# Kernel optimization log

Measured on AMD Instinct MI355X. Metric: run time of the kernel, lower is better.

## Reference

```python
import jax, jax.numpy as jnp
import numpy as np

D = 512      # embeddings_dim (in_features == out_features)
H = 4        # num_heads
MID = 2048   # mid_features
B, S = 4, 2048
EPS = 1e-5


def _ln(x, g, b):
    mu = jnp.mean(x, axis=-1, keepdims=True)
    var = jnp.mean(jnp.square(x - mu), axis=-1, keepdims=True)
    return g * (x - mu) / jnp.sqrt(var + EPS) + b


def setup_inputs() -> dict:
    key = jax.random.key(0)
    ks = jax.random.split(key, 16)
    w = 0.02  # weight init scale
    return {
        "x_encoder": jax.random.normal(ks[0], (B, S, D), jnp.float32),
        "x_decoder": jax.random.normal(ks[1], (B, S, D), jnp.float32),
        # per-head full-width projections (each head is a D->D Linear)
        "Wq": jax.random.normal(ks[2], (H, D, D), jnp.float32) * w,
        "bq": jnp.zeros((H, D), jnp.float32),
        "Wk": jax.random.normal(ks[3], (H, D, D), jnp.float32) * w,
        "bk": jnp.zeros((H, D), jnp.float32),
        "Wv": jax.random.normal(ks[4], (H, D, D), jnp.float32) * w,
        "bv": jnp.zeros((H, D), jnp.float32),
        # out_reshaper: Rearrange('b h s d -> b s (d h)') then Linear(D*H -> D)
        "Wo": jax.random.normal(ks[5], (D * H, D), jnp.float32) * w,
        "bo": jnp.zeros((D,), jnp.float32),
        "ln1_g": jnp.ones((D,), jnp.float32), "ln1_b": jnp.zeros((D,), jnp.float32),
        "ln2_g": jnp.ones((D,), jnp.float32), "ln2_b": jnp.zeros((D,), jnp.float32),
        # FouriFeedForward: D -> MID -> D with SELU
        "W1": jax.random.normal(ks[6], (D, MID), jnp.float32) * w,
        "b1": jnp.zeros((MID,), jnp.float32),
        "W2": jax.random.normal(ks[7], (MID, D), jnp.float32) * w,
        "b2": jnp.zeros((D,), jnp.float32),
        "ln3_g": jnp.ones((D,), jnp.float32), "ln3_b": jnp.zeros((D,), jnp.float32),
    }


def reference(x_encoder, x_decoder, Wq, bq, Wk, bk, Wv, bv, Wo, bo,
              ln1_g, ln1_b, ln2_g, ln2_b, W1, b1, W2, b2, ln3_g, ln3_b):
    # Fourier token mixing: per-batch fftn over (seq, feature) dims, keep real part
    xf = jnp.fft.fftn(x_decoder, axes=(1, 2)).real
    xd = _ln(x_decoder + xf, ln1_g, ln1_b)  # [B,S,D]

    # Linear multi-head attention: q from decoder, k/v from encoder.
    # qs/ks/vs: [B,H,S,D]; softmax over the HEAD axis (dim=1 in torch)
    qs = jax.nn.softmax(jnp.einsum('bsd,hde->bhse', xd, Wq) + bq[None, :, None, :], axis=1)
    ks = jax.nn.softmax(jnp.einsum('bsd,hde->bhse', x_encoder, Wk) + bk[None, :, None, :], axis=1)
    vs = jnp.einsum('bsd,hde->bhse', x_encoder, Wv) + bv[None, :, None, :]

    gc = jnp.einsum('bhsd,bhse->bhde', ks, vs)       # [B,H,D,D] global contexts
    out = jnp.einsum('bhsd,bhde->bhse', qs, gc)      # [B,H,S,D]

    # Rearrange 'b h s d -> b s (d h)': d is the slow axis, h the fast axis
    b, h, s, d = out.shape
    out = out.transpose(0, 2, 3, 1).reshape(b, s, d * h)
    attn = out @ Wo + bo                              # [B,S,D]

    x = _ln(xd + attn, ln2_g, ln2_b)
    ff = jax.nn.selu(x @ W1 + b1) @ W2 + b2           # dropout_p=0 (eval)
    x = _ln(x + ff, ln3_g, ln3_b)
    return x
```

## Files before the change

### kernel.cpp

```cpp
#include <hip/hip_runtime.h>
#include <stdint.h>

typedef __bf16 bf16;
typedef __bf16 bf16x8 __attribute__((ext_vector_type(8)));
typedef float f32x4 __attribute__((ext_vector_type(4)));

static __device__ __forceinline__ void async16(const void* g, void* l) {
  __builtin_amdgcn_global_load_lds(
      (__attribute__((address_space(1))) void*)g,
      (__attribute__((address_space(3))) void*)l, 16, 0, 0);
}

__global__ void __launch_bounds__(256) prep_all(
    const float* __restrict__ xdec, const float* __restrict__ xenc,
    bf16* __restrict__ Ttrig, bf16* __restrict__ Atrig2,
    bf16* __restrict__ xdec_b, bf16* __restrict__ xenc_b,
    const float* __restrict__ Wq, const float* __restrict__ Wk,
    const float* __restrict__ Wv, const float* __restrict__ Wo,
    const float* __restrict__ W1, const float* __restrict__ W2,
    bf16* __restrict__ BtQ, bf16* __restrict__ BtK, bf16* __restrict__ BtV,
    bf16* __restrict__ WoTh, bf16* __restrict__ W1T, bf16* __restrict__ W2T) {
  __shared__ bf16 tile[32][33];
  int id = blockIdx.x;
  if (id < 512) {
    int idx = id * 256 + threadIdx.x;
    int d0 = (idx & 127) * 4, jp = idx >> 7;
    int jj = jp >> 1, p = jp & 1;
    bf16 o[4] __attribute__((aligned(8)));
#pragma unroll
    for (int i = 0; i < 4; ++i) {
      int tt = ((d0 + i) * jj) & 511;
      float ang = (float)tt * (6.283185307179586f / 512.0f);
      o[i] = (bf16)(p ? __sinf(ang) : __cosf(ang));
    }
    *(uint2*)(Ttrig + jp * 512 + d0) = *(const uint2*)o;
  } else if (id < 2960) {
    int idx = (id - 512) * 256 + threadIdx.x;
    int k0 = (idx % 272) * 4;
    int rr = idx / 272;
    int r = rr % 1152, half = rr / 1152;
    bf16 o[4] __attribute__((aligned(8)));
#pragma unroll
    for (int i = 0; i < 4; ++i) {
      int k = k0 + i;
      float v = 0.0f;
      int tt = (r * k) & 2047;
      float ang = (float)tt * (6.283185307179586f / 2048.0f);
      if (half == 0) { if (r <= 1024 && k <= 1024) v = __cosf(ang); }
      else           { if (r <= 1023 && k >= 1 && k <= 1023) v = -__sinf(ang); }
      o[i] = (bf16)v;
    }
    *(uint2*)(Atrig2 + (long)rr * 1088 + k0) = *(const uint2*)o;
  } else if (id < 7056) {
    int i = ((id - 2960) * 256 + threadIdx.x) * 4;
    float4 v = *(const float4*)(xdec + i);
    bf16 o[4] __attribute__((aligned(8))) =
        {(bf16)v.x, (bf16)v.y, (bf16)v.z, (bf16)v.w};
    *(uint2*)(xdec_b + i) = *(const uint2*)o;
  } else if (id < 11152) {
    int i = ((id - 7056) * 256 + threadIdx.x) * 4;
    float4 v = *(const float4*)(xenc + i);
    bf16 o[4] __attribute__((aligned(8))) =
        {(bf16)v.x, (bf16)v.y, (bf16)v.z, (bf16)v.w};
    *(uint2*)(xenc_b + i) = *(const uint2*)o;
  } else {
    int id2 = id - 11152;
    int kind = id2 >> 10, t = id2 & 1023;
    const float* in; bf16* out; int R, C, rt, ct;
    bool iperm = false, hsel = false; int hh = 0;
    if (kind == 0)      { in = Wq; out = BtQ; R = 2048; C = 512; rt = t >> 4; ct = t & 15; iperm = true; }
    else if (kind == 1) { in = Wk; out = BtK; R = 2048; C = 512; rt = t >> 4; ct = t & 15; iperm = true; }
    else if (kind == 2) { in = Wv; out = BtV; R = 2048; C = 512; rt = t >> 4; ct = t & 15; iperm = true; }
    else if (kind == 3) {
      int zz = t >> 8, tt = t & 255;
      in = Wo; out = WoTh + (long)zz * 262144;
      R = 512; C = 512; rt = tt >> 4; ct = tt & 15; hsel = true; hh = zz;
    }
    else if (kind == 4) { in = W1; out = W1T; R = 512; C = 2048; rt = t >> 6; ct = t & 63; }
    else                { in = W2; out = W2T; R = 2048; C = 512; rt = t >> 4; ct = t & 15; }
    int c0 = ct * 32, r0 = rt * 32;
    int tx = threadIdx.x & 31, ty = threadIdx.x >> 5;
#pragma unroll
    for (int i = 0; i < 32; i += 8) {
      int r = r0 + ty + i;
      int rr = hsel ? (4 * r + hh) : r;
      tile[ty + i][tx] = (bf16)in[(long)rr * C + (c0 + tx)];
    }
    __syncthreads();
#pragma unroll
    for (int i = 0; i < 32; i += 8) {
      int cc = c0 + ty + i, rr = r0 + tx;
      if (iperm) {
        int e = cc, h = rr >> 9;
        int n = (e & 15) | (h << 4) | ((e >> 4) << 6);
        out[((long)n << 9) + (rr & 511)] = tile[tx][ty + i];
      } else {
        out[(long)cc * R + rr] = tile[tx][ty + i];
      }
    }
  }
}

__global__ void __launch_bounds__(256) fold_y(const bf16* __restrict__ Yt,
                                              bf16* __restrict__ Yf2) {
  int idx = blockIdx.x * 256 + threadIdx.x;
  int k0 = (idx % 272) * 4;
  int rr = idx / 272;
  int j = rr & 511, z = rr >> 9;
  int b = z & 3, half = z >> 2;
  const bf16* yin = Yt + (long)b * 2097152 + (long)j * 4096;
  bf16 o[4] __attribute__((aligned(8)));
  if (half == 0) {
    bf16 f[4] __attribute__((aligned(8)));
    *(uint2*)f = *(const uint2*)(yin + k0);
#pragma unroll
    for (int i = 0; i < 4; ++i) {
      int k = k0 + i;
      float v;
      if (k == 0)            v = (float)f[0];
      else if (k == 1024)    v = (float)f[i];
      else if (k < 1024)     v = (float)f[i] + (float)yin[2048 - k];
      else                   v = 0.0f;
      o[i] = (bf16)v;
    }
  } else {
    bf16 f[4] __attribute__((aligned(8)));
    *(uint2*)f = *(const uint2*)(yin + 2048 + k0);
#pragma unroll
    for (int i = 0; i < 4; ++i) {
      int k = k0 + i;
      float v = 0.0f;
      if (k >= 1 && k <= 1023) v = (float)f[i] - (float)yin[4096 - k];
      o[i] = (bf16)v;
    }
  }
  *(uint2*)(Yf2 + (long)z * 557056 + (long)j * 1088 + k0) = *(const uint2*)o;
}

__global__ void __launch_bounds__(256) ln1_kernel(
    const float* __restrict__ xdec, const bf16* __restrict__ CSb,
    const float* __restrict__ g, const float* __restrict__ be,
    bf16* __restrict__ outb) {
  const int row = blockIdx.x, t = threadIdx.x;
  const int b = row >> 11, s = row & 2047;
  const int sp = (s <= 1024) ? s : 2048 - s;
  const float sgn = (s <= 1024) ? 1.0f : -1.0f;
  const bf16* Crow = CSb + ((long)b * 1152 + sp) * 512;
  const bf16* Srow = CSb + ((long)(b + 4) * 1152 + sp) * 512;
  const long base = (long)row * 512;
  float2 xp = *(const float2*)(xdec + base + 2 * t);
  bf16 cp[2] __attribute__((aligned(4)));
  bf16 spv[2] __attribute__((aligned(4)));
  *(uint*)cp = *(const uint*)(Crow + 2 * t);
  *(uint*)spv = *(const uint*)(Srow + 2 * t);
  float v0 = xp.x + (float)cp[0] + sgn * (float)spv[0];
  float v1 = xp.y + (float)cp[1] + sgn * (float)spv[1];
  float sm = v0 + v1, q = v0 * v0 + v1 * v1;
#pragma unroll
  for (int off = 32; off > 0; off >>= 1) {
    sm += __shfl_down(sm, off);
    q += __shfl_down(q, off);
  }
  __shared__ float red[8];
  const int wv = t >> 6, ln = t & 63;
  if (ln == 0) { red[wv] = sm; red[wv + 4] = q; }
  __syncthreads();
  float S = red[0] + red[1] + red[2] + red[3];
  float Q = red[4] + red[5] + red[6] + red[7];
  float mu = S * (1.0f / 512.0f);
  float var = Q * (1.0f / 512.0f) - mu * mu;
  float rstd = rsqrtf(var + 1e-5f);
  float2 gp = *(const float2*)(g + 2 * t);
  float2 bp = *(const float2*)(be + 2 * t);
  bf16 op[2] __attribute__((aligned(4)));
  op[0] = (bf16)(gp.x * (v0 - mu) * rstd + bp.x);
  op[1] = (bf16)(gp.y * (v1 - mu) * rstd + bp.y);
  *(uint*)(outb + base + 2 * t) = *(const uint*)op;
}

template <int WRITE_BF16, int WRITE_F32>
__global__ void __launch_bounds__(256) ln_kernel(
    const bf16* __restrict__ A, const bf16* __restrict__ Bv,
    const float* __restrict__ g, const float* __restrict__ be,
    bf16* __restrict__ outb, float* __restrict__ outf) {
  const int row = blockIdx.x, t = threadIdx.x;
  const long base = (long)row * 512;
  bf16 ap[2] __attribute__((aligned(4)));
  bf16 bpv[2] __attribute__((aligned(4)));
  *(uint*)ap = *(const uint*)(A + base + 2 * t);
  *(uint*)bpv = *(const uint*)(Bv + base + 2 * t);
  float v0 = (float)ap[0] + (float)bpv[0];
  float v1 = (float)ap[1] + (float)bpv[1];
  float s = v0 + v1, q = v0 * v0 + v1 * v1;
#pragma unroll
  for (int off = 32; off > 0; off >>= 1) {
    s += __shfl_down(s, off);
    q += __shfl_down(q, off);
  }
  __shared__ float red[8];
  const int wv = t >> 6, ln = t & 63;
  if (ln == 0) { red[wv] = s; red[wv + 4] = q; }
  __syncthreads();
  float S = red[0] + red[1] + red[2] + red[3];
  float Q = red[4] + red[5] + red[6] + red[7];
  float mu = S * (1.0f / 512.0f);
  float var = Q * (1.0f / 512.0f) - mu * mu;
  float rstd = rsqrtf(var + 1e-5f);
  float2 gp = *(const float2*)(g + 2 * t);
  float2 bp = *(const float2*)(be + 2 * t);
  float o0 = gp.x * (v0 - mu) * rstd + bp.x;
  float o1 = gp.y * (v1 - mu) * rstd + bp.y;
  if (WRITE_BF16) {
    bf16 op[2] __attribute__((aligned(4)));
    op[0] = (bf16)o0; op[1] = (bf16)o1;
    *(uint*)(outb + base + 2 * t) = *(const uint*)op;
  }
  if (WRITE_F32) {
    float2 of; of.x = o0; of.y = o1;
    *(float2*)(outf + base + 2 * t) = of;
  }
}

template <int BN, int ADDR_MODE, int HAS_BIAS, int DO_SELU, int F32OUT, int SWIZ,
          int AHEAD>
static __device__ __forceinline__ void gemm_bt_body(
    int id, bf16* lA, bf16* lB,
    const bf16* __restrict__ A, const bf16* __restrict__ Bt,
    const float* __restrict__ bias, void* __restrict__ Cout,
    int N, int K, long sAz, long sBz, long sBiasz, long sCz,
    int gx, int gy, int gin) {
  int x, y, z;
  {
    if (SWIZ == 0) {
      x = id % gx; int t2 = id / gx; y = t2 % gy; z = t2 / gy;
    } else {
      int xcd = id & 7, r = id >> 3;
      int inner = r % gin, G = xcd + 8 * (r / gin);
      if (SWIZ == 1)      { y = G; x = inner % gx; z = inner / gx; }
      else if (SWIZ == 2) { z = G; x = inner % gx; y = inner / gx; }
      else                { x = G; y = inner % gy; z = inner / gy; }
    }
  }
  A  += (AHEAD == 1) ? sAz * (z & 3) : (AHEAD == 2) ? sAz * (z >> 2) : sAz * z;
  Bt += sBz * z;
  const int m0 = y * 128, n0 = x * BN;
  const int t = threadIdx.x;
  const int lane = t & 63, wave = t >> 6;
  const int srow = t >> 3;
  const int pch  = t & 7;
  const int lch  = pch ^ (srow & 7);
  const bf16* Ag = A  + (long)(m0 + srow) * K + lch * 8;
  const bf16* Bg = Bt + (long)(n0 + srow) * K + lch * 8;
  bf16* lAp = lA + srow * 64 + pch * 8;
  bf16* lBp = lB + srow * 64 + pch * 8;
  constexpr int MI = (BN == 128) ? 4 : 2;
  const int wm = (BN == 128) ? (wave >> 1) * 64 : wave * 32;
  const int wn = (BN == 128) ? (wave & 1) * 64 : 0;
  const int fr = lane & 15, fq = lane >> 4;

  f32x4 acc[MI][4] = {};

  for (int k0 = 0; k0 < K; k0 += 64) {
    __syncthreads();
#pragma unroll
    for (int i = 0; i < 4; ++i)
      async16(Ag + k0 + (long)(32 * i) * K, lAp + 32 * i * 64);
#pragma unroll
    for (int i = 0; i < BN / 32; ++i)
      async16(Bg + k0 + (long)(32 * i) * K, lBp + 32 * i * 64);
    __syncthreads();
#pragma unroll
    for (int kk = 0; kk < 2; ++kk) {
      bf16x8 av[MI], bfrag[4];
#pragma unroll
      for (int mi = 0; mi < MI; ++mi) {
        int r = wm + mi * 16 + fr;
        int c = (kk * 4 + fq) ^ (r & 7);
        av[mi] = *(const bf16x8*)&lA[r * 64 + c * 8];
      }
#pragma unroll
      for (int ni = 0; ni < 4; ++ni) {
        int r = wn + ni * 16 + fr;
        int c = (kk * 4 + fq) ^ (r & 7);
        bfrag[ni] = *(const bf16x8*)&lB[r * 64 + c * 8];
      }
#pragma unroll
      for (int mi = 0; mi < MI; ++mi)
#pragma unroll
        for (int ni = 0; ni < 4; ++ni)
          acc[mi][ni] = __builtin_amdgcn_mfma_f32_16x16x32_bf16(
              av[mi], bfrag[ni], acc[mi][ni], 0, 0, 0);
    }
  }

#pragma unroll
  for (int mi = 0; mi < MI; ++mi) {
#pragma unroll
    for (int ni = 0; ni < 4; ++ni) {
      const int col = n0 + wn + ni * 16 + fr;
      float bias_v = 0.0f;
      if (HAS_BIAS == 1) bias_v = bias[sBiasz * z + col];
      if (ADDR_MODE == 9) {
        const int b = z >> 2, h = z & 3;
        const int kidx = (col & 15) | (h << 4) | ((col >> 4) << 6);
#pragma unroll
        for (int r = 0; r < 4; ++r) {
          const int row = m0 + wm + mi * 16 + fq * 4 + r;
          ((bf16*)Cout)[((long)(b * 512 + row)) * 2048 + kidx] =
              (bf16)(acc[mi][ni][r] + bias_v);
        }
      } else {
#pragma unroll
        for (int r = 0; r < 4; ++r) {
          const int row = m0 + wm + mi * 16 + fq * 4 + r;
          float v = acc[mi][ni][r] + bias_v;
          if (DO_SELU) v = v > 0.0f ? 1.0507009873554805f * v
                                    : 1.7580993408473766f * (__expf(v) - 1.0f);
          long addr = sCz * z + (long)row * N + col;
          if (F32OUT) ((float*)Cout)[addr] = v;
          else        ((bf16*)Cout)[addr] = (bf16)v;
        }
      }
    }
  }
}

template <int BN, int ADDR_MODE, int HAS_BIAS, int DO_SELU, int F32OUT, int SWIZ,
          int AHEAD = 0>
__global__ void __launch_bounds__(256, 2) gemm_bt(
    const bf16* __restrict__ A, const bf16* __restrict__ Bt,
    const float* __restrict__ bias, void* __restrict__ Cout,
    int N, int K, long sAz, long sBz, long sBiasz, long sCz,
    int gx, int gy, int gin) {
  __shared__ __align__(16) bf16 lA[128 * 64];
  __shared__ __align__(16) bf16 lB[BN * 64];
  gemm_bt_body<BN, ADDR_MODE, HAS_BIAS, DO_SELU, F32OUT, SWIZ, AHEAD>(
      blockIdx.x, lA, lB, A, Bt, bias, Cout, N, K, sAz, sBz, sBiasz, sCz, gx, gy, gin);
}

static __device__ __forceinline__ void qkv_body(
    int id, bf16* lA, bf16* lB,
    const bf16* __restrict__ Aq, const bf16* __restrict__ Aenc,
    const bf16* __restrict__ BQ, const bf16* __restrict__ BK,
    const bf16* __restrict__ BV,
    const float* __restrict__ bq, const float* __restrict__ bk,
    const float* __restrict__ bv,
    bf16* __restrict__ qs2, bf16* __restrict__ ksT, bf16* __restrict__ vsT) {
  const int sid = id & 1023;
  const int xcd = sid & 7, r = sid >> 3;
  const int x = r & 15, y = xcd + 8 * (r >> 4);
  const bf16 *A = Aq, *Bt = BQ; bf16* out = qs2; const float* bias = bq;
  (void)Aenc; (void)BK; (void)BV; (void)bk; (void)bv; (void)ksT; (void)vsT;
  const int K = 512;
  const int m0 = y * 128, n0 = x * 128;
  const int t = threadIdx.x;
  const int lane = t & 63, wave = t >> 6;
  const int srow = t >> 3, pch = t & 7, lch = pch ^ (srow & 7);
  const bf16* Ag = A  + (long)(m0 + srow) * K + lch * 8;
  const bf16* Bg = Bt + (long)(n0 + srow) * K + lch * 8;
  bf16* lAp = lA + srow * 64 + pch * 8;
  bf16* lBp = lB + srow * 64 + pch * 8;
  const int wm = (wave >> 1) * 64, wn = (wave & 1) * 64;
  const int fr = lane & 15, fq = lane >> 4;

  f32x4 acc[4][4] = {};
  for (int k0 = 0; k0 < K; k0 += 64) {
    __syncthreads();
#pragma unroll
    for (int i = 0; i < 4; ++i) {
      async16(Ag + k0 + (long)(32 * i) * K, lAp + 32 * i * 64);
      async16(Bg + k0 + (long)(32 * i) * K, lBp + 32 * i * 64);
    }
    __syncthreads();
#pragma unroll
    for (int kk = 0; kk < 2; ++kk) {
      bf16x8 av[4], bfrag[4];
#pragma unroll
      for (int mi = 0; mi < 4; ++mi) {
        int rr = wm + mi * 16 + fr;
        int c = (kk * 4 + fq) ^ (rr & 7);
        av[mi] = *(const bf16x8*)&lA[rr * 64 + c * 8];
      }
#pragma unroll
      for (int ni = 0; ni < 4; ++ni) {
        int rr = wn + ni * 16 + fr;
        int c = (kk * 4 + fq) ^ (rr & 7);
        bfrag[ni] = *(const bf16x8*)&lB[rr * 64 + c * 8];
      }
#pragma unroll
      for (int mi = 0; mi < 4; ++mi)
#pragma unroll
        for (int ni = 0; ni < 4; ++ni)
          acc[mi][ni] = __builtin_amdgcn_mfma_f32_16x16x32_bf16(
              av[mi], bfrag[ni], acc[mi][ni], 0, 0, 0);
    }
  }

  const int ebase = fr + 16 * ((n0 + wn) >> 6);
  const float b0 = bias[ebase], b1 = bias[512 + ebase],
              b2 = bias[1024 + ebase], b3 = bias[1536 + ebase];
#pragma unroll
  for (int mi = 0; mi < 4; ++mi) {
#pragma unroll
    for (int r = 0; r < 4; ++r) {
      const int row = m0 + wm + mi * 16 + fq * 4 + r;
      float v0 = acc[mi][0][r] + b0;
      float v1 = acc[mi][1][r] + b1;
      float v2 = acc[mi][2][r] + b2;
      float v3 = acc[mi][3][r] + b3;
      float m = fmaxf(fmaxf(v0, v1), fmaxf(v2, v3));
      float p0 = __expf(v0 - m), p1 = __expf(v1 - m),
            p2 = __expf(v2 - m), p3 = __expf(v3 - m);
      float rs = 1.0f / (p0 + p1 + p2 + p3);
      const long ob = (long)row * 2048 + n0 + wn + fr;
      out[ob]      = (bf16)(p0 * rs);
      out[ob + 16] = (bf16)(p1 * rs);
      out[ob + 32] = (bf16)(p2 * rs);
      out[ob + 48] = (bf16)(p3 * rs);
    }
  }
}

static __device__ __forceinline__ void kv2_body(
    int sid, bf16* smem,
    const bf16* __restrict__ Aenc, const bf16* __restrict__ BK,
    const bf16* __restrict__ BV,
    const float* __restrict__ bk, const float* __restrict__ bv,
    bf16* __restrict__ ksT, bf16* __restrict__ vsT) {
  const int xcd = sid & 7, r = sid >> 3;
  const int x = r & 15, y = xcd + 8 * (r >> 4);
  const int K = 512;
  const int m0 = y * 128, n0 = x * 128;
  const int t = threadIdx.x;
  const int lane = t & 63, wave = t >> 6;
  const int srow = t >> 3, pch = t & 7, lch = pch ^ (srow & 7);
  bf16* lA  = smem;
  bf16* lBK = smem + 8192;
  bf16* lBV = smem + 16384;
  const bf16* Ag  = Aenc + (long)(m0 + srow) * K + lch * 8;
  const bf16* BKg = BK   + (long)(n0 + srow) * K + lch * 8;
  const bf16* BVg = BV   + (long)(n0 + srow) * K + lch * 8;
  bf16* lAp  = lA  + srow * 64 + pch * 8;
  bf16* lBKp = lBK + srow * 64 + pch * 8;
  bf16* lBVp = lBV + srow * 64 + pch * 8;
  const int wm = (wave >> 1) * 64, wn = (wave & 1) * 64;
  const int fr = lane & 15, fq = lane >> 4;

  f32x4 accK[4][4] = {}, accV[4][4] = {};
  for (int k0 = 0; k0 < K; k0 += 64) {
    __syncthreads();
#pragma unroll
    for (int i = 0; i < 4; ++i) {
      async16(Ag  + k0 + (long)(32 * i) * K, lAp  + 32 * i * 64);
      async16(BKg + k0 + (long)(32 * i) * K, lBKp + 32 * i * 64);
      async16(BVg + k0 + (long)(32 * i) * K, lBVp + 32 * i * 64);
    }
    __syncthreads();
#pragma unroll
    for (int kk = 0; kk < 2; ++kk) {
      bf16x8 av[4], bkf[4], bvf[4];
#pragma unroll
      for (int mi = 0; mi < 4; ++mi) {
        int rr = wm + mi * 16 + fr;
        int c = (kk * 4 + fq) ^ (rr & 7);
        av[mi] = *(const bf16x8*)&lA[rr * 64 + c * 8];
      }
#pragma unroll
      for (int ni = 0; ni < 4; ++ni) {
        int rr = wn + ni * 16 + fr;
        int c = (kk * 4 + fq) ^ (rr & 7);
        bkf[ni] = *(const bf16x8*)&lBK[rr * 64 + c * 8];
        bvf[ni] = *(const bf16x8*)&lBV[rr * 64 + c * 8];
      }
#pragma unroll
      for (int mi = 0; mi < 4; ++mi)
#pragma unroll
        for (int ni = 0; ni < 4; ++ni) {
          accK[mi][ni] = __builtin_amdgcn_mfma_f32_16x16x32_bf16(
              av[mi], bkf[ni], accK[mi][ni], 0, 0, 0);
          accV[mi][ni] = __builtin_amdgcn_mfma_f32_16x16x32_bf16(
              av[mi], bvf[ni], accV[mi][ni], 0, 0, 0);
        }
    }
  }

  const int ebase = fr + 16 * ((n0 + wn) >> 6);
  const float kb0 = bk[ebase], kb1 = bk[512 + ebase],
              kb2 = bk[1024 + ebase], kb3 = bk[1536 + ebase];
  const float vb0 = bv[ebase], vb1 = bv[512 + ebase],
              vb2 = bv[1024 + ebase], vb3 = bv[1536 + ebase];
  bf16* lT = smem;
  const int bb = m0 >> 11;
  const int s_tile = m0 & 2047;
  const int e_loc = fr + 16 * (wn >> 6);
  const int c = lane & 15, rg = lane >> 4;

  __syncthreads();
#pragma unroll
  for (int mi = 0; mi < 4; ++mi) {
    const int s0 = wm + mi * 16 + fq * 4;
    bf16 tmp[4][4] __attribute__((aligned(8)));
#pragma unroll
    for (int r2 = 0; r2 < 4; ++r2) {
      float v0 = accK[mi][0][r2] + kb0;
      float v1 = accK[mi][1][r2] + kb1;
      float v2 = accK[mi][2][r2] + kb2;
      float v3 = accK[mi][3][r2] + kb3;
      float m = fmaxf(fmaxf(v0, v1), fmaxf(v2, v3));
      float p0 = __expf(v0 - m), p1 = __expf(v1 - m),
            p2 = __expf(v2 - m), p3 = __expf(v3 - m);
      float rs = 1.0f / (p0 + p1 + p2 + p3);
      tmp[0][r2] = (bf16)(p0 * rs); tmp[1][r2] = (bf16)(p1 * rs);
      tmp[2][r2] = (bf16)(p2 * rs); tmp[3][r2] = (bf16)(p3 * rs);
    }
#pragma unroll
    for (int ni = 0; ni < 4; ++ni) {
      const int row = ni * 32 + e_loc;
      const int el = row * 128 + ((((s0 >> 3) ^ (row & 15)) << 3) | (s0 & 7));
      *(uint2*)&lT[el] = *(const uint2*)tmp[ni];
    }
  }
  __syncthreads();
#pragma unroll
  for (int i = 0; i < 8; ++i) {
    const int row = wave * 32 + rg + i * 4;
    const int el = row * 128 + ((c ^ (row & 15)) << 3);
    uint4 v = *(const uint4*)&lT[el];
    const int h = row >> 5, e = (row & 31) + 32 * x;
    *(uint4*)(ksT + ((long)((bb * 4 + h) * 512 + e)) * 2048 + s_tile + c * 8) = v;
  }

  __syncthreads();
#pragma unroll
  for (int mi = 0; mi < 4; ++mi) {
    const int s0 = wm + mi * 16 + fq * 4;
    bf16 tmp[4][4] __attribute__((aligned(8)));
#pragma unroll
    for (int r2 = 0; r2 < 4; ++r2) {
      tmp[0][r2] = (bf16)(accV[mi][0][r2] + vb0);
      tmp[1][r2] = (bf16)(accV[mi][1][r2] + vb1);
      tmp[2][r2] = (bf16)(accV[mi][2][r2] + vb2);
      tmp[3][r2] = (bf16)(accV[mi][3][r2] + vb3);
    }
#pragma unroll
    for (int ni = 0; ni < 4; ++ni) {
      const int row = ni * 32 + e_loc;
      const int el = row * 128 + ((((s0 >> 3) ^ (row & 15)) << 3) | (s0 & 7));
      *(uint2*)&lT[el] = *(const uint2*)tmp[ni];
    }
  }
  __syncthreads();
#pragma unroll
  for (int i = 0; i < 8; ++i) {
    const int row = wave * 32 + rg + i * 4;
    const int el = row * 128 + ((c ^ (row & 15)) << 3);
    uint4 v = *(const uint4*)&lT[el];
    const int h = row >> 5, e = (row & 31) + 32 * x;
    *(uint4*)(vsT + ((long)((bb * 4 + h) * 512 + e)) * 2048 + s_tile + c * 8) = v;
  }
}

__global__ void __launch_bounds__(256, 2) fused_kv_yt(
    const bf16* __restrict__ Aenc, const bf16* __restrict__ BK,
    const bf16* __restrict__ BV,
    const float* __restrict__ bk, const float* __restrict__ bv,
    bf16* __restrict__ ksT, bf16* __restrict__ vsT,
    const bf16* __restrict__ Ttrig, const bf16* __restrict__ xdec_b,
    bf16* __restrict__ Yt) {
  __shared__ __align__(16) bf16 smem[24576];
  int id = blockIdx.x;
  if (id < 1024)
    kv2_body(id, smem, Aenc, BK, BV, bk, bv, ksT, vsT);
  else
    gemm_bt_body<128, 0, 0, 0, 0, 3, 0>(id - 1024, smem, smem + 8192,
        Ttrig, xdec_b, nullptr, Yt, 2048, 512, 0L, 1048576L, 0L, 2097152L, 16, 8, 32);
}

__global__ void __launch_bounds__(256, 2) fused_gc_cs(
    const bf16* __restrict__ ksT, const bf16* __restrict__ vsT,
    bf16* __restrict__ gc,
    const bf16* __restrict__ Atrig2, const bf16* __restrict__ Yf2,
    bf16* __restrict__ CSb) {
  __shared__ __align__(16) bf16 smem[12288];
  int id = blockIdx.x;
  if (id < 512)
    gemm_bt_body<64, 0, 0, 0, 0, 2, 0>(id, smem, smem + 8192,
        ksT, vsT, nullptr, gc, 512, 2048, 1048576L, 1048576L, 0L, 262144L, 8, 4, 32);
  else
    gemm_bt_body<64, 0, 0, 0, 0, 2, 2>(id - 512, smem, smem + 8192,
        Atrig2, Yf2, nullptr, CSb, 512, 1088, 1253376L, 557056L, 0L, 589824L, 8, 9, 72);
}

__global__ void __launch_bounds__(256, 2) fused_q_gw(
    const bf16* __restrict__ Aq, const bf16* __restrict__ BQ,
    const float* __restrict__ bq, bf16* __restrict__ qs2,
    const bf16* __restrict__ WoTh, const bf16* __restrict__ gc,
    bf16* __restrict__ gwT) {
  __shared__ __align__(16) bf16 smem[16384];
  int id = blockIdx.x;
  if (id < 1024)
    qkv_body(id, smem, smem + 8192, Aq, nullptr, BQ, nullptr, nullptr,
             bq, nullptr, nullptr, qs2, nullptr, nullptr);
  else
    gemm_bt_body<64, 9, 0, 0, 0, 2, 1>(id - 1024, smem, smem + 8192,
        WoTh, gc, nullptr, gwT, 512, 512, 262144L, 262144L, 0L, 0L, 8, 4, 32);
}

extern "C" void kernel_launch(void* const* d_in, const int* in_sizes, int n_in,
                              void* d_out, int out_size, void* d_ws, size_t ws_size,
                              hipStream_t stream) {
  (void)in_sizes; (void)n_in; (void)out_size; (void)ws_size;
  const float* x_enc = (const float*)d_in[0];
  const float* x_dec = (const float*)d_in[1];
  const float* Wq = (const float*)d_in[2];
  const float* bq = (const float*)d_in[3];
  const float* Wk = (const float*)d_in[4];
  const float* bk = (const float*)d_in[5];
  const float* Wv = (const float*)d_in[6];
  const float* bv = (const float*)d_in[7];
  const float* Wo = (const float*)d_in[8];
  const float* bo = (const float*)d_in[9];
  const float* g1 = (const float*)d_in[10];
  const float* be1 = (const float*)d_in[11];
  const float* g2 = (const float*)d_in[12];
  const float* be2 = (const float*)d_in[13];
  const float* W1 = (const float*)d_in[14];
  const float* b1 = (const float*)d_in[15];
  const float* W2 = (const float*)d_in[16];
  const float* b2 = (const float*)d_in[17];
  const float* g3 = (const float*)d_in[18];
  const float* be3 = (const float*)d_in[19];

  char* ws = (char*)d_ws;
  const size_t MB = 1u << 20;
  bf16*  BtQ    = (bf16*) (ws + 0);
  bf16*  midb   = (bf16*) (ws + 0);
  bf16*  ksT    = (bf16*) (ws + 32 * MB);
  bf16*  attn_b = (bf16*) (ws + 32 * MB);
  bf16*  vsT    = (bf16*) (ws + 64 * MB);
  bf16*  ff_b   = (bf16*) (ws + 72 * MB);
  bf16*  Atrig2 = (bf16*) (ws + 96 * MB);
  bf16*  Ttrig  = (bf16*) (ws + 101 * MB);
  bf16*  CSb    = (bf16*) (ws + 102 * MB);
  bf16*  qs2    = (bf16*) (ws + 96 * MB);
  bf16*  xenc_b = (bf16*) (ws + 128 * MB);
  bf16*  BtK    = (bf16*) (ws + 136 * MB);
  bf16*  BtV    = (bf16*) (ws + 138 * MB);
  bf16*  xd_b   = (bf16*) (ws + 192 * MB);
  bf16*  x2_b   = (bf16*) (ws + 200 * MB);
  bf16*  gwT    = (bf16*) (ws + 208 * MB);
  bf16*  Yt     = (bf16*) (ws + 216 * MB);
  bf16*  gc     = (bf16*) (ws + 216 * MB);
  bf16*  Yf2    = (bf16*) (ws + 232 * MB);
  bf16*  WoTh   = (bf16*) (ws + 241 * MB);
  bf16*  W1T    = (bf16*) (ws + 243 * MB);
  bf16*  W2T    = (bf16*) (ws + 245 * MB);
  bf16*  xdec_b = (bf16*) (ws + 247 * MB);

  prep_all<<<17296, 256, 0, stream>>>(x_dec, x_enc, Ttrig, Atrig2, xdec_b, xenc_b,
                                      Wq, Wk, Wv, Wo, W1, W2,
                                      BtQ, BtK, BtV, WoTh, W1T, W2T);

  fused_kv_yt<<<1536, 256, 0, stream>>>(xenc_b, BtK, BtV, bk, bv, ksT, vsT,
                                        Ttrig, xdec_b, Yt);

  fold_y<<<4352, 256, 0, stream>>>(Yt, Yf2);

  fused_gc_cs<<<1088, 256, 0, stream>>>(ksT, vsT, gc, Atrig2, Yf2, CSb);

  ln1_kernel<<<8192, 256, 0, stream>>>(x_dec, CSb, g1, be1, xd_b);

  fused_q_gw<<<1536, 256, 0, stream>>>(xd_b, BtQ, bq, qs2, WoTh, gc, gwT);

  gemm_bt<64, 0, 1, 0, 0, 1><<<512, 256, 0, stream>>>(
      qs2, gwT, bo, attn_b, 512, 2048, 4194304L, 1048576L, 0L, 1048576L, 8, 16, 32);
  ln_kernel<1, 0><<<8192, 256, 0, stream>>>(
      xd_b, attn_b, g2, be2, x2_b, nullptr);

  gemm_bt<128, 0, 1, 1, 0, 1><<<1024, 256, 0, stream>>>(
      x2_b, W1T, b1, midb, 2048, 512, 0L, 0L, 0L, 0L, 16, 64, 16);
  gemm_bt<64, 0, 1, 0, 0, 1><<<512, 256, 0, stream>>>(
      midb, W2T, b2, ff_b, 512, 2048, 0L, 0L, 0L, 0L, 8, 64, 8);
  ln_kernel<0, 1><<<8192, 256, 0, stream>>>(
      x2_b, ff_b, g3, be3, nullptr, (float*)d_out);
}
```

Measured before the change: 355.6 us.

## Split-K the two K=2048 output GEMMs and sum the partials in LayerNorm

Replaces the attention output projection and FFN down-projection GEMMs (K=2048, N=512) with a split-K kernel. It uses 128x128 tiles, divides K into two halves and writes fp32 partial sums to two buffers. The following LayerNorm kernels read both partials and add them to the residual, so no separate reduction pass is needed. The aim is more work per block and better CU utilisation on a small N. The cost is extra fp32 write and read traffic and uncoalesced scalar stores in the epilogue.

```diff
diff --git a/kernel.cpp b/kernel.cpp
--- a/kernel.cpp
+++ b/kernel.cpp
@@ -179,18 +179,19 @@
 }
 
 template <int WRITE_BF16, int WRITE_F32>
-__global__ void __launch_bounds__(256) ln_kernel(
-    const bf16* __restrict__ A, const bf16* __restrict__ Bv,
+__global__ void __launch_bounds__(256) ln_sum2(
+    const bf16* __restrict__ A, const float* __restrict__ P0,
+    const float* __restrict__ P1,
     const float* __restrict__ g, const float* __restrict__ be,
     bf16* __restrict__ outb, float* __restrict__ outf) {
   const int row = blockIdx.x, t = threadIdx.x;
   const long base = (long)row * 512;
   bf16 ap[2] __attribute__((aligned(4)));
-  bf16 bpv[2] __attribute__((aligned(4)));
   *(uint*)ap = *(const uint*)(A + base + 2 * t);
-  *(uint*)bpv = *(const uint*)(Bv + base + 2 * t);
-  float v0 = (float)ap[0] + (float)bpv[0];
-  float v1 = (float)ap[1] + (float)bpv[1];
+  float2 p0 = *(const float2*)(P0 + base + 2 * t);
+  float2 p1 = *(const float2*)(P1 + base + 2 * t);
+  float v0 = (float)ap[0] + p0.x + p1.x;
+  float v1 = (float)ap[1] + p0.y + p1.y;
   float s = v0 + v1, q = v0 * v0 + v1 * v1;
 #pragma unroll
   for (int off = 32; off > 0; off >>= 1) {
@@ -338,19 +339,106 @@
       blockIdx.x, lA, lB, A, Bt, bias, Cout, N, K, sAz, sBz, sBiasz, sCz, gx, gy, gin);
 }
 
+template <int Z4>
+__global__ void __launch_bounds__(256, 2) gemm_sk2(
+    const bf16* __restrict__ A, const bf16* __restrict__ Bt,
+    const float* __restrict__ bias,
+    float* __restrict__ P0, float* __restrict__ P1,
+    long sAz, long sBz) {
+  __shared__ __align__(16) bf16 lA[128 * 64];
+  __shared__ __align__(16) bf16 lB[2][64 * 64];
+  const int id = blockIdx.x;
+  const int xcd = id & 7, r = id >> 3;
+  const int xp = r & 3;
+  int y, z, ks;
+  if (Z4) { z = xcd >> 1; ks = xcd & 1; y = r >> 2; }
+  else    { z = 0; ks = xcd & 1; y = (xcd >> 1) * 16 + (r >> 2); }
+  const int K = 2048, KH = 1024;
+  A  += (long)z * sAz + (long)ks * KH;
+  Bt += (long)z * sBz + (long)ks * KH;
+  const int m0 = y * 128, n0 = xp * 128;
+  const int t = threadIdx.x;
+  const int lane = t & 63, wave = t >> 6;
+  const int srow = t >> 3, pch = t & 7, lch = pch ^ (srow & 7);
+  const bf16* Ag  = A  + (long)(m0 + srow) * K + lch * 8;
+  const bf16* B0g = Bt + (long)(n0 + srow) * K + lch * 8;
+  const bf16* B1g = Bt + (long)(n0 + 64 + srow) * K + lch * 8;
+  bf16* lAp  = lA + srow * 64 + pch * 8;
+  bf16* lB0p = lB[0] + srow * 64 + pch * 8;
+  bf16* lB1p = lB[1] + srow * 64 + pch * 8;
+  const int wm = wave * 32;
+  const int fr = lane & 15, fq = lane >> 4;
+
+  f32x4 acc[2][2][4] = {};
+  for (int k0 = 0; k0 < KH; k0 += 64) {
+    __syncthreads();
+#pragma unroll
+    for (int i = 0; i < 4; ++i)
+      async16(Ag + k0 + (long)(32 * i) * K, lAp + 32 * i * 64);
+#pragma unroll
+    for (int i = 0; i < 2; ++i) {
+      async16(B0g + k0 + (long)(32 * i) * K, lB0p + 32 * i * 64);
+      async16(B1g + k0 + (long)(32 * i) * K, lB1p + 32 * i * 64);
+    }
+    __syncthreads();
+#pragma unroll
+    for (int kk = 0; kk < 2; ++kk) {
+      bf16x8 av[2];
+#pragma unroll
+      for (int mi = 0; mi < 2; ++mi) {
+        int rr = wm + mi * 16 + fr;
+        int c = (kk * 4 + fq) ^ (rr & 7);
+        av[mi] = *(const bf16x8*)&lA[rr * 64 + c * 8];
+      }
+#pragma unroll
+      for (int s = 0; s < 2; ++s) {
+        bf16x8 bfrag[4];
+#pragma unroll
+        for (int ni = 0; ni < 4; ++ni) {
+          int rr = ni * 16 + fr;
+          int c = (kk * 4 + fq) ^ (rr & 7);
+          bfrag[ni] = *(const bf16x8*)&lB[s][rr * 64 + c * 8];
+        }
+#pragma unroll
+        for (int mi = 0; mi < 2; ++mi)
+#pragma unroll
+          for (int ni = 0; ni < 4; ++ni)
+            acc[s][mi][ni] = __builtin_amdgcn_mfma_f32_16x16x32_bf16(
+                av[mi], bfrag[ni], acc[s][mi][ni], 0, 0, 0);
+      }
+    }
+  }
+
+  float* P = ks ? P1 : P0;
+#pragma unroll
+  for (int s = 0; s < 2; ++s) {
+#pragma unroll
+    for (int mi = 0; mi < 2; ++mi) {
+#pragma unroll
+      for (int ni = 0; ni < 4; ++ni) {
+        const int col = n0 + s * 64 + ni * 16 + fr;
+        const float bias_v = (ks == 0) ? bias[col] : 0.0f;
+#pragma unroll
+        for (int r2 = 0; r2 < 4; ++r2) {
+          const int row = m0 + wm + mi * 16 + fq * 4 + r2;
+          const long addr = ((long)(Z4 ? z * 2048 + row : row)) * 512 + col;
+          P[addr] = acc[s][mi][ni][r2] + bias_v;
+        }
+      }
+    }
+  }
+}
+
 static __device__ __forceinline__ void qkv_body(
     int id, bf16* lA, bf16* lB,
-    const bf16* __restrict__ Aq, const bf16* __restrict__ Aenc,
-    const bf16* __restrict__ BQ, const bf16* __restrict__ BK,
-    const bf16* __restrict__ BV,
-    const float* __restrict__ bq, const float* __restrict__ bk,
-    const float* __restrict__ bv,
-    bf16* __restrict__ qs2, bf16* __restrict__ ksT, bf16* __restrict__ vsT) {
+    const bf16* __restrict__ Aq,
+    const bf16* __restrict__ BQ,
+    const float* __restrict__ bq,
+    bf16* __restrict__ qs2) {
   const int sid = id & 1023;
   const int xcd = sid & 7, r = sid >> 3;
   const int x = r & 15, y = xcd + 8 * (r >> 4);
   const bf16 *A = Aq, *Bt = BQ; bf16* out = qs2; const float* bias = bq;
-  (void)Aenc; (void)BK; (void)BV; (void)bk; (void)bv; (void)ksT; (void)vsT;
   const int K = 512;
   const int m0 = y * 128, n0 = x * 128;
   const int t = threadIdx.x;
@@ -599,8 +687,7 @@
   __shared__ __align__(16) bf16 smem[16384];
   int id = blockIdx.x;
   if (id < 1024)
-    qkv_body(id, smem, smem + 8192, Aq, nullptr, BQ, nullptr, nullptr,
-             bq, nullptr, nullptr, qs2, nullptr, nullptr);
+    qkv_body(id, smem, smem + 8192, Aq, BQ, bq, qs2);
   else
     gemm_bt_body<64, 9, 0, 0, 0, 2, 1>(id - 1024, smem, smem + 8192,
         WoTh, gc, nullptr, gwT, 512, 512, 262144L, 262144L, 0L, 0L, 8, 4, 32);
@@ -636,14 +723,16 @@
   bf16*  BtQ    = (bf16*) (ws + 0);
   bf16*  midb   = (bf16*) (ws + 0);
   bf16*  ksT    = (bf16*) (ws + 32 * MB);
-  bf16*  attn_b = (bf16*) (ws + 32 * MB);
+  float* aP0    = (float*)(ws + 32 * MB);
+  float* aP1    = (float*)(ws + 48 * MB);
   bf16*  vsT    = (bf16*) (ws + 64 * MB);
-  bf16*  ff_b   = (bf16*) (ws + 72 * MB);
   bf16*  Atrig2 = (bf16*) (ws + 96 * MB);
   bf16*  Ttrig  = (bf16*) (ws + 101 * MB);
   bf16*  CSb    = (bf16*) (ws + 102 * MB);
   bf16*  qs2    = (bf16*) (ws + 96 * MB);
   bf16*  xenc_b = (bf16*) (ws + 128 * MB);
+  float* wP0    = (float*)(ws + 128 * MB);
+  float* wP1    = (float*)(ws + 144 * MB);
   bf16*  BtK    = (bf16*) (ws + 136 * MB);
   bf16*  BtV    = (bf16*) (ws + 138 * MB);
   bf16*  xd_b   = (bf16*) (ws + 192 * MB);
@@ -672,15 +761,13 @@
 
   fused_q_gw<<<1536, 256, 0, stream>>>(xd_b, BtQ, bq, qs2, WoTh, gc, gwT);
 
-  gemm_bt<64, 0, 1, 0, 0, 1><<<512, 256, 0, stream>>>(
-      qs2, gwT, bo, attn_b, 512, 2048, 4194304L, 1048576L, 0L, 1048576L, 8, 16, 32);
-  ln_kernel<1, 0><<<8192, 256, 0, stream>>>(
-      xd_b, attn_b, g2, be2, x2_b, nullptr);
+  gemm_sk2<1><<<512, 256, 0, stream>>>(qs2, gwT, bo, aP0, aP1,
+                                       4194304L, 1048576L);
+  ln_sum2<1, 0><<<8192, 256, 0, stream>>>(xd_b, aP0, aP1, g2, be2, x2_b, nullptr);
 
   gemm_bt<128, 0, 1, 1, 0, 1><<<1024, 256, 0, stream>>>(
       x2_b, W1T, b1, midb, 2048, 512, 0L, 0L, 0L, 0L, 16, 64, 16);
-  gemm_bt<64, 0, 1, 0, 0, 1><<<512, 256, 0, stream>>>(
-      midb, W2T, b2, ff_b, 512, 2048, 0L, 0L, 0L, 0L, 8, 64, 8);
-  ln_kernel<0, 1><<<8192, 256, 0, stream>>>(
-      x2_b, ff_b, g3, be3, nullptr, (float*)d_out);
-}
+  gemm_sk2<0><<<512, 256, 0, stream>>>(midb, W2T, b2, wP0, wP1, 0L, 0L);
+  ln_sum2<0, 1><<<8192, 256, 0, stream>>>(x2_b, wP0, wP1, g3, be3, nullptr,
+                                          (float*)d_out);
+}
```

After: 356.8 us. No clear change (+0.3%).
